# Performance work log

Measured on AMD Instinct MI355X. Metric: run time of the kernel, lower is better.

Reference implementation:

```python
import jax, jax.numpy as jnp
import numpy as np

EPS = 1e-5


def setup_inputs() -> dict:
    key = jax.random.key(0)
    ks = jax.random.split(key, 4)
    b, c, h, w = 4, 256, 64, 64
    x = jax.random.normal(ks[0], (b, c, h, w), dtype=jnp.float32)
    W_qkv = jax.random.normal(ks[1], (3 * c, c), dtype=jnp.float32) * (1.0 / np.sqrt(c))
    b_qkv = jnp.zeros((3 * c,), dtype=jnp.float32)
    W_out = jax.random.normal(ks[2], (c, c), dtype=jnp.float32) * (1.0 / np.sqrt(c))
    b_out = jnp.zeros((c,), dtype=jnp.float32)
    gamma = jnp.ones((c,), dtype=jnp.float32)
    beta = jnp.zeros((c,), dtype=jnp.float32)
    return {"x": x, "W_qkv": W_qkv, "b_qkv": b_qkv, "W_out": W_out,
            "b_out": b_out, "gamma": gamma, "beta": beta}


def reference(x, W_qkv, b_qkv, W_out, b_out, gamma, beta):
    b, c, h, w = x.shape
    n = h * w  # number of spatial tokens

    # BatchNorm2d (training mode: batch statistics over b,h,w per channel)
    mean = jnp.mean(x, axis=(0, 2, 3), keepdims=True)
    var = jnp.var(x, axis=(0, 2, 3), keepdims=True)
    x_norm = (x - mean) * jax.lax.rsqrt(var + EPS)
    x_norm = x_norm * gamma[None, :, None, None] + beta[None, :, None, None]

    # 1x1 conv to QKV: [b, 3c, h, w]
    qkv = jnp.einsum('bchw,oc->bohw', x_norm, W_qkv) + b_qkv[None, :, None, None]
    q, k, v = jnp.split(qkv, 3, axis=1)

    q = q.transpose(0, 2, 3, 1).reshape(b, n, c)  # [b, n, c]
    k = k.reshape(b, c, n)                         # [b, c, n]
    v = v.transpose(0, 2, 3, 1).reshape(b, n, c)  # [b, n, c]

    scale = c ** (-0.5)
    dot = jnp.einsum('bqc,bck->bqk', q, k) * scale  # [b, n, n]
    attn = jax.nn.softmax(dot, axis=-1)
    out = jnp.einsum('bqk,bkc->bqc', attn, v)       # [b, n, c]
    out = out.reshape(b, h, w, c).transpose(0, 3, 1, 2)  # [b, c, h, w]

    # 1x1 output conv + residual
    out = jnp.einsum('bchw,oc->bohw', out, W_out) + b_out[None, :, None, None]
    return out + x
```

## Files before the change

kernel.cpp:

```cpp
#include <hip/hip_runtime.h>
#include <hip/hip_bf16.h>

typedef __attribute__((ext_vector_type(4))) float f32x4;
typedef __attribute__((ext_vector_type(8))) short bf16x8;
typedef __attribute__((ext_vector_type(4))) unsigned int u32x4;

#define BB 4
#define C 256
#define N 4096
#define TS 32
#define EPSI 1e-5f

constexpr size_t BBNC = (size_t)BB * N * C;

__device__ __forceinline__ unsigned short f2bf(float f) {
    unsigned int u = __builtin_bit_cast(unsigned int, f);
    u += 0x7fffu + ((u >> 16) & 1u);
    return (unsigned short)(u >> 16);
}

__device__ __forceinline__ float bf2f(unsigned short h) {
    unsigned int u = ((unsigned int)h) << 16;
    return __builtin_bit_cast(float, u);
}

__device__ __forceinline__ unsigned int cvt_pk_bf16(float lo, float hi) {
    unsigned int r;
    asm("v_cvt_pk_bf16_f32 %0, %1, %2" : "=v"(r) : "v"(lo), "v"(hi));
    return r;
}

__device__ __forceinline__ void stage16(const unsigned short* g, unsigned short* l) {
    __builtin_amdgcn_global_load_lds(
        (const __attribute__((address_space(1))) void*)g,
        (__attribute__((address_space(3))) void*)l, 16, 0, 0);
}

__global__ __launch_bounds__(256) void bn_stats_k(
    const float* __restrict__ x, const float* __restrict__ gamma,
    const float* __restrict__ beta, float* __restrict__ scale, float* __restrict__ shift,
    const float* __restrict__ Wqkv, unsigned short* __restrict__ wqkv_bf)
{
    int tid = threadIdx.x;
    if (blockIdx.x >= C) {
        size_t i = ((size_t)(blockIdx.x - C) * 256 + tid);
        const float4* p = (const float4*)(Wqkv + i * 8);
        float4 a = p[0], c = p[1];
        unsigned int pk[4];
        pk[0] = cvt_pk_bf16(a.x, a.y);
        pk[1] = cvt_pk_bf16(a.z, a.w);
        pk[2] = cvt_pk_bf16(c.x, c.y);
        pk[3] = cvt_pk_bf16(c.z, c.w);
        *(u32x4*)(wqkv_bf + i * 8) = *(u32x4*)pk;
        return;
    }
    int c = blockIdx.x;
    float s = 0.f, s2 = 0.f;
    for (int b = 0; b < BB; ++b) {
        const float4* p = (const float4*)(x + ((size_t)b * C + c) * N);
        for (int i = tid; i < N / 4; i += 256) {
            float4 v = p[i];
            s  += v.x + v.y + v.z + v.w;
            s2 += v.x * v.x + v.y * v.y + v.z * v.z + v.w * v.w;
        }
    }
    for (int m = 1; m < 64; m <<= 1) {
        s  += __shfl_xor(s, m);
        s2 += __shfl_xor(s2, m);
    }
    __shared__ float rs[4], rs2[4];
    int w = tid >> 6;
    if ((tid & 63) == 0) { rs[w] = s; rs2[w] = s2; }
    __syncthreads();
    if (tid == 0) {
        float S  = rs[0] + rs[1] + rs[2] + rs[3];
        float S2 = rs2[0] + rs2[1] + rs2[2] + rs2[3];
        const float inv_n = 1.f / (BB * N);
        float mean = S * inv_n;
        float var  = S2 * inv_n - mean * mean;
        float sc = gamma[c] * rsqrtf(var + EPSI);
        scale[c] = sc;
        shift[c] = beta[c] - mean * sc;
    }
}

__global__ __launch_bounds__(256) void qkv_gemm_k(
    const float* __restrict__ x, const unsigned short* __restrict__ wqkv_bf,
    const float* __restrict__ bqkv,
    const float* __restrict__ scale, const float* __restrict__ shift,
    unsigned short* __restrict__ q, unsigned short* __restrict__ kt, unsigned short* __restrict__ v)
{
    __shared__ unsigned short Alds[32 * 264];
    __shared__ unsigned short Wlds[64 * 256];

    int tid = threadIdx.x;
    int b  = blockIdx.y;
    int T0 = blockIdx.x * 32;
    int lane = tid & 63;
    int w = tid >> 6;
    int wm = w >> 1, wn = w & 1;
    int g = lane >> 4, l15 = lane & 15;

    {
        int cbase = tid >> 1;
        int t0 = (tid & 1) * 16;
#pragma unroll
        for (int pass = 0; pass < 2; ++pass) {
            int cc = cbase + pass * 128;
            const float4* xp = (const float4*)(x + ((size_t)b * C + cc) * N + T0 + t0);
            float sc = scale[cc], sh = shift[cc];
#pragma unroll
            for (int j = 0; j < 4; ++j) {
                float4 vv = xp[j];
                int t = t0 + j * 4;
                Alds[(t + 0) * 264 + cc] = f2bf(vv.x * sc + sh);
                Alds[(t + 1) * 264 + cc] = f2bf(vv.y * sc + sh);
                Alds[(t + 2) * 264 + cc] = f2bf(vv.z * sc + sh);
                Alds[(t + 3) * 264 + cc] = f2bf(vv.w * sc + sh);
            }
        }
    }

    const float QSCALE = 0.0625f * 1.44269504088896f;

    for (int oi = 0; oi < 12; ++oi) {
        int O0 = oi * 64;
        __syncthreads();
        {
            const unsigned short* wb = wqkv_bf + (size_t)O0 * 256;
#pragma unroll
            for (int j = 0; j < 8; ++j) {
                int qq = tid + j * 256;
                int lo = qq >> 5, sc2 = qq & 31;
                stage16(wb + (size_t)lo * 256 + ((sc2 ^ (lo & 7)) * 8), &Wlds[qq * 8]);
            }
        }
        __syncthreads();

        f32x4 acc[2];
        acc[0] = f32x4{0.f, 0.f, 0.f, 0.f};
        acc[1] = f32x4{0.f, 0.f, 0.f, 0.f};
#pragma unroll
        for (int kk = 0; kk < 8; ++kk) {
            bf16x8 afr = *(const bf16x8*)&Alds[(wm * 16 + l15) * 264 + kk * 32 + g * 8];
#pragma unroll
            for (int nf = 0; nf < 2; ++nf) {
                int lo = wn * 32 + nf * 16 + l15;
                bf16x8 bfr = *(const bf16x8*)&Wlds[lo * 256 + (((kk * 4 + g) ^ (lo & 7)) * 8)];
                acc[nf] = __builtin_amdgcn_mfma_f32_16x16x32_bf16(afr, bfr, acc[nf], 0, 0, 0);
            }
        }

#pragma unroll
        for (int nf = 0; nf < 2; ++nf) {
            int o = O0 + wn * 32 + nf * 16 + l15;
            float bias = bqkv[o];
#pragma unroll
            for (int r = 0; r < 4; ++r) {
                int t = T0 + wm * 16 + g * 4 + r;
                float val = acc[nf][r] + bias;
                if (O0 < 256) {
                    q[((size_t)b * N + t) * C + o] = f2bf(val * QSCALE);
                } else if (O0 < 512) {
                    kt[((size_t)b * N + t) * C + (o - 256)] = f2bf(val);
                } else {
                    int tp = (t & ~31) | ((g * 2 + wm) * 4 + r);
                    v[((size_t)b * C + (o - 512)) * N + tp] = f2bf(val);
                }
            }
        }
    }
}

template<int NSEG>
__global__ __launch_bounds__(256, 2) void attn_k(
    const unsigned short* __restrict__ q, const unsigned short* __restrict__ kt,
    const unsigned short* __restrict__ v,
    unsigned short* __restrict__ P, float* __restrict__ ml)
{
    constexpr int NS  = N / NSEG;
    constexpr int NIT = NS / TS;
    __shared__ unsigned short Klds[2][TS * 256];
    __shared__ unsigned short Vlds[2][256 * TS];

    int tid = threadIdx.x;
    int h  = blockIdx.y;
    int b  = blockIdx.z;
    int Q0 = blockIdx.x * 128;
    int lane = tid & 63;
    int lw = tid >> 6;
    int g = lane >> 4, l15 = lane & 15;

    bf16x8 qf[2][8];
#pragma unroll
    for (int m = 0; m < 2; ++m) {
        const unsigned short* qp = q + ((size_t)b * N + Q0 + lw * 32 + m * 16 + l15) * C + g * 8;
#pragma unroll
        for (int kc = 0; kc < 8; ++kc)
            qf[m][kc] = *(const bf16x8*)(qp + kc * 32);
    }

    f32x4 oacc[2][16];
#pragma unroll
    for (int m = 0; m < 2; ++m)
#pragma unroll
        for (int i = 0; i < 16; ++i) oacc[m][i] = f32x4{0.f, 0.f, 0.f, 0.f};
    float mrow[2] = {-1e30f, -1e30f};
    float lg[2]   = {0.f, 0.f};

    const unsigned short* kb = kt + ((size_t)b * N + h * NS) * C;
    const unsigned short* vb = v + (size_t)b * C * N + h * NS;

#define STAGE(buf_, t_)                                                              \
    {                                                                                \
        const unsigned short* kbt = kb + (size_t)(t_) * TS * 256;                    \
        _Pragma("unroll")                                                            \
        for (int j = 0; j < 4; ++j) {                                                \
            int qq = tid + j * 256;                                                  \
            int tk = qq >> 5, sc = qq & 31;                                          \
            stage16(kbt + tk * 256 + ((sc ^ (tk & 7)) * 8), &Klds[buf_][qq * 8]);    \
        }                                                                            \
        _Pragma("unroll")                                                            \
        for (int j = 0; j < 4; ++j) {                                                \
            int qq = tid + j * 256;                                                  \
            int c = qq >> 2, sl = qq & 3;                                            \
            stage16(vb + (size_t)c * N + (t_) * TS + ((sl ^ ((c >> 1) & 3)) * 8),    \
                    &Vlds[buf_][qq * 8]);                                            \
        }                                                                            \
    }

    STAGE(0, 0);
    __syncthreads();

    for (int t = 0; t < NIT; ++t) {
        int cur = t & 1;
        if (t < NIT - 1) STAGE(cur ^ 1, t + 1);

        f32x4 st[2][2];
#pragma unroll
        for (int m = 0; m < 2; ++m)
#pragma unroll
            for (int ct = 0; ct < 2; ++ct) st[m][ct] = f32x4{0.f, 0.f, 0.f, 0.f};
        __builtin_amdgcn_s_setprio(1);
#pragma unroll
        for (int kc = 0; kc < 8; ++kc) {
#pragma unroll
            for (int ct = 0; ct < 2; ++ct) {
                int tk = ct * 16 + l15;
                int slot = (kc * 4 + g) ^ (tk & 7);
                bf16x8 kf = *(const bf16x8*)&Klds[cur][tk * 256 + slot * 8];
                st[0][ct] = __builtin_amdgcn_mfma_f32_16x16x32_bf16(kf, qf[0][kc], st[0][ct], 0, 0, 0);
                st[1][ct] = __builtin_amdgcn_mfma_f32_16x16x32_bf16(kf, qf[1][kc], st[1][ct], 0, 0, 0);
            }
        }
        __builtin_amdgcn_s_setprio(0);

        float mx[2];
#pragma unroll
        for (int m = 0; m < 2; ++m)
            mx[m] = fmaxf(fmaxf(fmaxf(st[m][0][0], st[m][0][1]), fmaxf(st[m][0][2], st[m][0][3])),
                          fmaxf(fmaxf(st[m][1][0], st[m][1][1]), fmaxf(st[m][1][2], st[m][1][3])));
        bool ok = (mx[0] - mrow[0] <= 8.f) & (mx[1] - mrow[1] <= 8.f);
        if (!__all(ok)) {
#pragma unroll
            for (int m = 0; m < 2; ++m) {
                float v0 = mx[m];
                v0 = fmaxf(v0, __shfl_xor(v0, 16));
                v0 = fmaxf(v0, __shfl_xor(v0, 32));
                float mn = fmaxf(mrow[m], v0);
                float alpha = exp2f(mrow[m] - mn);
                mrow[m] = mn;
                lg[m] *= alpha;
#pragma unroll
                for (int f = 0; f < 16; ++f)
#pragma unroll
                    for (int r = 0; r < 4; ++r) oacc[m][f][r] *= alpha;
            }
        }
        bf16x8 pf[2];
#pragma unroll
        for (int m = 0; m < 2; ++m) {
            float rs = 0.f;
#pragma unroll
            for (int ct = 0; ct < 2; ++ct)
#pragma unroll
                for (int r = 0; r < 4; ++r) {
                    float p = exp2f(st[m][ct][r] - mrow[m]);
                    st[m][ct][r] = p;
                    rs += p;
                }
            lg[m] += rs;
            u32x4 pk;
            pk[0] = cvt_pk_bf16(st[m][0][0], st[m][0][1]);
            pk[1] = cvt_pk_bf16(st[m][0][2], st[m][0][3]);
            pk[2] = cvt_pk_bf16(st[m][1][0], st[m][1][1]);
            pk[3] = cvt_pk_bf16(st[m][1][2], st[m][1][3]);
            pf[m] = __builtin_bit_cast(bf16x8, pk);
        }

        __builtin_amdgcn_s_setprio(1);
#pragma unroll
        for (int cf = 0; cf < 16; ++cf) {
            int c = cf * 16 + l15;
            int vslot = g ^ ((c >> 1) & 3);
            bf16x8 vf = *(const bf16x8*)&Vlds[cur][c * TS + vslot * 8];
            oacc[0][cf] = __builtin_amdgcn_mfma_f32_16x16x32_bf16(vf, pf[0], oacc[0][cf], 0, 0, 0);
            oacc[1][cf] = __builtin_amdgcn_mfma_f32_16x16x32_bf16(vf, pf[1], oacc[1][cf], 0, 0, 0);
        }
        __builtin_amdgcn_s_setprio(0);
        __syncthreads();
    }

    float lt[2];
#pragma unroll
    for (int m = 0; m < 2; ++m) {
        float v0 = lg[m];
        v0 += __shfl_xor(v0, 16);
        v0 += __shfl_xor(v0, 32);
        lt[m] = v0;
    }
#pragma unroll
    for (int m = 0; m < 2; ++m) {
        size_t tokid = (size_t)b * N + Q0 + lw * 32 + m * 16 + l15;
        if (g == 0) {
            ml[(size_t)(2 * h + 0) * (BB * N) + tokid] = mrow[m];
            ml[(size_t)(2 * h + 1) * (BB * N) + tokid] = lt[m];
        }
        unsigned short* pp = P + (size_t)h * BBNC + tokid * C;
#pragma unroll
        for (int cf = 0; cf < 16; ++cf) {
#pragma unroll
            for (int rp = 0; rp < 2; ++rp) {
                int c = cf * 16 + g * 4 + rp * 2;
                unsigned int pk2 = cvt_pk_bf16(oacc[m][cf][rp * 2 + 0], oacc[m][cf][rp * 2 + 1]);
                *(unsigned int*)&pp[c] = pk2;
            }
        }
    }
}

template<int NSEG>
__global__ __launch_bounds__(256) void out_gemm_k(
    const unsigned short* __restrict__ P, const float* __restrict__ ml,
    const float* __restrict__ Wout, const float* __restrict__ bout,
    const float* __restrict__ x, float* __restrict__ out)
{
    __shared__ unsigned short Alds[256 * 40];
    __shared__ unsigned short Blds[32 * 40];

    int tid = threadIdx.x;
    int b  = blockIdx.y;
    int T0 = blockIdx.x * 32;
    int lane = tid & 63;
    int w = tid >> 6;
    int g = lane >> 4, l15 = lane & 15;

    int tl = (tid >> 2) & 31;
    float cw[NSEG], cinv;
    {
        size_t tok = (size_t)b * N + T0 + tl;
        float ms[NSEG], ls[NSEG];
#pragma unroll
        for (int s = 0; s < NSEG; ++s) {
            ms[s] = ml[(size_t)(2 * s + 0) * (BB * N) + tok];
            ls[s] = ml[(size_t)(2 * s + 1) * (BB * N) + tok];
        }
        float M = ms[0];
#pragma unroll
        for (int s = 1; s < NSEG; ++s) M = fmaxf(M, ms[s]);
        float den = 0.f;
#pragma unroll
        for (int s = 0; s < NSEG; ++s) {
            cw[s] = exp2f(ms[s] - M);
            den += cw[s] * ls[s];
        }
        cinv = 1.f / den;
    }

    f32x4 acc[4][2];
#pragma unroll
    for (int i = 0; i < 4; ++i)
#pragma unroll
        for (int j = 0; j < 2; ++j) acc[i][j] = f32x4{0.f, 0.f, 0.f, 0.f};

    for (int c0 = 0; c0 < C; c0 += 32) {
        if (c0) __syncthreads();
        {
            const float4* wp = (const float4*)(Wout + (size_t)tid * C + c0);
            unsigned int wpk[16];
#pragma unroll
            for (int j = 0; j < 8; ++j) {
                float4 vv = wp[j];
                wpk[2 * j + 0] = cvt_pk_bf16(vv.x, vv.y);
                wpk[2 * j + 1] = cvt_pk_bf16(vv.z, vv.w);
            }
#pragma unroll
            for (int j = 0; j < 16; ++j)
                *(unsigned int*)&Alds[tid * 40 + j * 2] = wpk[j];
        }
        if (tid < 128) {
            int j = tid & 3;
            size_t base = ((size_t)b * N + T0 + tl) * C + c0 + j * 8;
            float val[8];
#pragma unroll
            for (int e = 0; e < 8; ++e) val[e] = 0.f;
#pragma unroll
            for (int s = 0; s < NSEG; ++s) {
                bf16x8 p = *(const bf16x8*)(P + (size_t)s * BBNC + base);
                float wgt = cw[s];
#pragma unroll
                for (int e = 0; e < 8; ++e) val[e] += wgt * bf2f((unsigned short)p[e]);
            }
            unsigned int opk[4];
#pragma unroll
            for (int jj = 0; jj < 4; ++jj)
                opk[jj] = cvt_pk_bf16(val[2 * jj] * cinv, val[2 * jj + 1] * cinv);
            *(u32x4*)&Blds[tl * 40 + j * 8] = *(u32x4*)opk;
        }
        __syncthreads();

        bf16x8 afr[4];
#pragma unroll
        for (int mf = 0; mf < 4; ++mf)
            afr[mf] = *(const bf16x8*)&Alds[(w * 64 + mf * 16 + l15) * 40 + g * 8];
#pragma unroll
        for (int tf = 0; tf < 2; ++tf) {
            bf16x8 bfr = *(const bf16x8*)&Blds[(tf * 16 + l15) * 40 + g * 8];
#pragma unroll
            for (int mf = 0; mf < 4; ++mf)
                acc[mf][tf] = __builtin_amdgcn_mfma_f32_16x16x32_bf16(afr[mf], bfr, acc[mf][tf], 0, 0, 0);
        }
    }

#pragma unroll
    for (int mf = 0; mf < 4; ++mf) {
#pragma unroll
        for (int tf = 0; tf < 2; ++tf) {
            int t = T0 + tf * 16 + l15;
#pragma unroll
            for (int r = 0; r < 4; ++r) {
                int co = w * 64 + mf * 16 + g * 4 + r;
                size_t oidx = ((size_t)b * C + co) * N + t;
                out[oidx] = acc[mf][tf][r] + bout[co] + x[oidx];
            }
        }
    }
}

extern "C" void kernel_launch(void* const* d_in, const int* in_sizes, int n_in,
                              void* d_out, int out_size, void* d_ws, size_t ws_size,
                              hipStream_t stream) {
    const float* x     = (const float*)d_in[0];
    const float* Wqkv  = (const float*)d_in[1];
    const float* bqkv  = (const float*)d_in[2];
    const float* Wout  = (const float*)d_in[3];
    const float* bout  = (const float*)d_in[4];
    const float* gamma = (const float*)d_in[5];
    const float* beta  = (const float*)d_in[6];
    float* out = (float*)d_out;

    char* ws = (char*)d_ws;
    float* scale = (float*)ws;
    float* shift = (float*)(ws + 1024);
    unsigned short* q  = (unsigned short*)(ws + 4096);
    unsigned short* kt = q  + BBNC;
    unsigned short* v  = kt + BBNC;
    unsigned short* P  = v  + BBNC;
    unsigned short* wqkv_bf = P;

    size_t need4 = 4096 + 7 * BBNC * 2 + (size_t)8 * BB * N * 4;

    bn_stats_k<<<dim3(C + 96), dim3(256), 0, stream>>>(x, gamma, beta, scale, shift, Wqkv, wqkv_bf);
    qkv_gemm_k<<<dim3(N / 32, BB), dim3(256), 0, stream>>>(x, wqkv_bf, bqkv, scale, shift, q, kt, v);

    if (ws_size >= need4) {
        float* ml = (float*)(P + 4 * BBNC);
        attn_k<4><<<dim3(N / 128, 4, BB), dim3(256), 0, stream>>>(q, kt, v, P, ml);
        out_gemm_k<4><<<dim3(N / 32, BB), dim3(256), 0, stream>>>(P, ml, Wout, bout, x, out);
    } else {
        float* ml = (float*)(P + 2 * BBNC);
        attn_k<2><<<dim3(N / 128, 2, BB), dim3(256), 0, stream>>>(q, kt, v, P, ml);
        out_gemm_k<2><<<dim3(N / 32, BB), dim3(256), 0, stream>>>(P, ml, Wout, bout, x, out);
    }
}
```

Baseline: 149.4 us.

## Software-pipeline PV MFMA behind next QK tile and pre-convert Wout to bf16

The attention loop now splits K and V staging and defers each tile's P·V matrix multiply to the next iteration, after that iteration's QK^T. The softmax exponentials can then overlap with the MFMA work, and the V load for tile t+1 is issued after the barrier. Separately, Wout is converted to bf16 once inside the BN-stats kernel rather than being re-converted from fp32 by every out_gemm block. This adds a workspace region for Wout and changes the barrier and staging order, which raises register pressure and the risk of synchronization mistakes.

Measured after the change: 152.3 us. 1.02x slower.

```diff
diff --git a/kernel.cpp b/kernel.cpp
--- a/kernel.cpp
+++ b/kernel.cpp
@@ -39,19 +39,25 @@
 __global__ __launch_bounds__(256) void bn_stats_k(
     const float* __restrict__ x, const float* __restrict__ gamma,
     const float* __restrict__ beta, float* __restrict__ scale, float* __restrict__ shift,
-    const float* __restrict__ Wqkv, unsigned short* __restrict__ wqkv_bf)
+    const float* __restrict__ Wqkv, unsigned short* __restrict__ wqkv_bf,
+    const float* __restrict__ Wout, unsigned short* __restrict__ wout_bf)
 {
     int tid = threadIdx.x;
     if (blockIdx.x >= C) {
-        size_t i = ((size_t)(blockIdx.x - C) * 256 + tid);
-        const float4* p = (const float4*)(Wqkv + i * 8);
+        int cb = blockIdx.x - C;
+        const float* src;
+        unsigned short* dst;
+        size_t i;
+        if (cb < 96) { src = Wqkv; dst = wqkv_bf; i = (size_t)cb * 256 + tid; }
+        else         { src = Wout; dst = wout_bf; i = (size_t)(cb - 96) * 256 + tid; }
+        const float4* p = (const float4*)(src + i * 8);
         float4 a = p[0], c = p[1];
         unsigned int pk[4];
         pk[0] = cvt_pk_bf16(a.x, a.y);
         pk[1] = cvt_pk_bf16(a.z, a.w);
         pk[2] = cvt_pk_bf16(c.x, c.y);
         pk[3] = cvt_pk_bf16(c.z, c.w);
-        *(u32x4*)(wqkv_bf + i * 8) = *(u32x4*)pk;
+        *(u32x4*)(dst + i * 8) = *(u32x4*)pk;
         return;
     }
     int c = blockIdx.x;
@@ -211,7 +217,7 @@
     const unsigned short* kb = kt + ((size_t)b * N + h * NS) * C;
     const unsigned short* vb = v + (size_t)b * C * N + h * NS;
 
-#define STAGE(buf_, t_)                                                              \
+#define STAGE_K(buf_, t_)                                                            \
     {                                                                                \
         const unsigned short* kbt = kb + (size_t)(t_) * TS * 256;                    \
         _Pragma("unroll")                                                            \
@@ -220,6 +226,9 @@
             int tk = qq >> 5, sc = qq & 31;                                          \
             stage16(kbt + tk * 256 + ((sc ^ (tk & 7)) * 8), &Klds[buf_][qq * 8]);    \
         }                                                                            \
+    }
+#define STAGE_V(buf_, t_)                                                            \
+    {                                                                                \
         _Pragma("unroll")                                                            \
         for (int j = 0; j < 4; ++j) {                                                \
             int qq = tid + j * 256;                                                  \
@@ -229,12 +238,15 @@
         }                                                                            \
     }
 
-    STAGE(0, 0);
+    STAGE_K(0, 0);
+    STAGE_V(0, 0);
     __syncthreads();
 
+    bf16x8 pf[2];
+
     for (int t = 0; t < NIT; ++t) {
-        int cur = t & 1;
-        if (t < NIT - 1) STAGE(cur ^ 1, t + 1);
+        int s = t & 1;
+        if (t + 1 < NIT) STAGE_K(s ^ 1, t + 1);
 
         f32x4 st[2][2];
 #pragma unroll
@@ -248,12 +260,25 @@
             for (int ct = 0; ct < 2; ++ct) {
                 int tk = ct * 16 + l15;
                 int slot = (kc * 4 + g) ^ (tk & 7);
-                bf16x8 kf = *(const bf16x8*)&Klds[cur][tk * 256 + slot * 8];
+                bf16x8 kf = *(const bf16x8*)&Klds[s][tk * 256 + slot * 8];
                 st[0][ct] = __builtin_amdgcn_mfma_f32_16x16x32_bf16(kf, qf[0][kc], st[0][ct], 0, 0, 0);
                 st[1][ct] = __builtin_amdgcn_mfma_f32_16x16x32_bf16(kf, qf[1][kc], st[1][ct], 0, 0, 0);
             }
         }
         __builtin_amdgcn_s_setprio(0);
+
+        if (t > 0) {
+            __builtin_amdgcn_s_setprio(1);
+#pragma unroll
+            for (int cf = 0; cf < 16; ++cf) {
+                int c = cf * 16 + l15;
+                int vslot = g ^ ((c >> 1) & 3);
+                bf16x8 vf = *(const bf16x8*)&Vlds[s ^ 1][c * TS + vslot * 8];
+                oacc[0][cf] = __builtin_amdgcn_mfma_f32_16x16x32_bf16(vf, pf[0], oacc[0][cf], 0, 0, 0);
+                oacc[1][cf] = __builtin_amdgcn_mfma_f32_16x16x32_bf16(vf, pf[1], oacc[1][cf], 0, 0, 0);
+            }
+            __builtin_amdgcn_s_setprio(0);
+        }
 
         float mx[2];
 #pragma unroll
@@ -277,7 +302,6 @@
                     for (int r = 0; r < 4; ++r) oacc[m][f][r] *= alpha;
             }
         }
-        bf16x8 pf[2];
 #pragma unroll
         for (int m = 0; m < 2; ++m) {
             float rs = 0.f;
@@ -298,17 +322,20 @@
             pf[m] = __builtin_bit_cast(bf16x8, pk);
         }
 
-        __builtin_amdgcn_s_setprio(1);
+        __syncthreads();
+        if (t + 1 < NIT) STAGE_V(s ^ 1, t + 1);
+    }
+
+    {
+        int s = (NIT - 1) & 1;
 #pragma unroll
         for (int cf = 0; cf < 16; ++cf) {
             int c = cf * 16 + l15;
             int vslot = g ^ ((c >> 1) & 3);
-            bf16x8 vf = *(const bf16x8*)&Vlds[cur][c * TS + vslot * 8];
+            bf16x8 vf = *(const bf16x8*)&Vlds[s][c * TS + vslot * 8];
             oacc[0][cf] = __builtin_amdgcn_mfma_f32_16x16x32_bf16(vf, pf[0], oacc[0][cf], 0, 0, 0);
             oacc[1][cf] = __builtin_amdgcn_mfma_f32_16x16x32_bf16(vf, pf[1], oacc[1][cf], 0, 0, 0);
         }
-        __builtin_amdgcn_s_setprio(0);
-        __syncthreads();
     }
 
     float lt[2];
@@ -342,7 +369,7 @@
 template<int NSEG>
 __global__ __launch_bounds__(256) void out_gemm_k(
     const unsigned short* __restrict__ P, const float* __restrict__ ml,
-    const float* __restrict__ Wout, const float* __restrict__ bout,
+    const unsigned short* __restrict__ wout_bf, const float* __restrict__ bout,
     const float* __restrict__ x, float* __restrict__ out)
 {
     __shared__ unsigned short Alds[256 * 40];
@@ -386,17 +413,10 @@
     for (int c0 = 0; c0 < C; c0 += 32) {
         if (c0) __syncthreads();
         {
-            const float4* wp = (const float4*)(Wout + (size_t)tid * C + c0);
-            unsigned int wpk[16];
-#pragma unroll
-            for (int j = 0; j < 8; ++j) {
-                float4 vv = wp[j];
-                wpk[2 * j + 0] = cvt_pk_bf16(vv.x, vv.y);
-                wpk[2 * j + 1] = cvt_pk_bf16(vv.z, vv.w);
-            }
-#pragma unroll
-            for (int j = 0; j < 16; ++j)
-                *(unsigned int*)&Alds[tid * 40 + j * 2] = wpk[j];
+            const unsigned short* wp = wout_bf + (size_t)tid * C + c0;
+#pragma unroll
+            for (int jj = 0; jj < 4; ++jj)
+                *(bf16x8*)&Alds[tid * 40 + jj * 8] = *(const bf16x8*)(wp + jj * 8);
         }
         if (tid < 128) {
             int j = tid & 3;
@@ -462,24 +482,26 @@
     char* ws = (char*)d_ws;
     float* scale = (float*)ws;
     float* shift = (float*)(ws + 1024);
-    unsigned short* q  = (unsigned short*)(ws + 4096);
+    unsigned short* wout_bf = (unsigned short*)(ws + 4096);
+    unsigned short* q  = wout_bf + (size_t)C * C;
     unsigned short* kt = q  + BBNC;
     unsigned short* v  = kt + BBNC;
     unsigned short* P  = v  + BBNC;
     unsigned short* wqkv_bf = P;
 
-    size_t need4 = 4096 + 7 * BBNC * 2 + (size_t)8 * BB * N * 4;
-
-    bn_stats_k<<<dim3(C + 96), dim3(256), 0, stream>>>(x, gamma, beta, scale, shift, Wqkv, wqkv_bf);
+    size_t need4 = 4096 + (size_t)C * C * 2 + 7 * BBNC * 2 + (size_t)8 * BB * N * 4;
+
+    bn_stats_k<<<dim3(C + 128), dim3(256), 0, stream>>>(x, gamma, beta, scale, shift,
+                                                        Wqkv, wqkv_bf, Wout, wout_bf);
     qkv_gemm_k<<<dim3(N / 32, BB), dim3(256), 0, stream>>>(x, wqkv_bf, bqkv, scale, shift, q, kt, v);
 
     if (ws_size >= need4) {
         float* ml = (float*)(P + 4 * BBNC);
         attn_k<4><<<dim3(N / 128, 4, BB), dim3(256), 0, stream>>>(q, kt, v, P, ml);
-        out_gemm_k<4><<<dim3(N / 32, BB), dim3(256), 0, stream>>>(P, ml, Wout, bout, x, out);
+        out_gemm_k<4><<<dim3(N / 32, BB), dim3(256), 0, stream>>>(P, ml, wout_bf, bout, x, out);
     } else {
         float* ml = (float*)(P + 2 * BBNC);
         attn_k<2><<<dim3(N / 128, 2, BB), dim3(256), 0, stream>>>(q, kt, v, P, ml);
-        out_gemm_k<2><<<dim3(N / 32, BB), dim3(256), 0, stream>>>(P, ml, Wout, bout, x, out);
-    }
-}
+        out_gemm_k<2><<<dim3(N / 32, BB), dim3(256), 0, stream>>>(P, ml, wout_bf, bout, x, out);
+    }
+}
```
